# Performance work log

Hardware: AMD Instinct MI355X
Metric: run time of the kernel (lower is better)

The kernel has to match this reference:

```python
import jax, jax.numpy as jnp
import numpy as np
from jax import lax

PRE_NMS_TOPK = 6000
POST_NMS_TOPK = 1000
NMS_THRESH = 0.7
MIN_SIZE = 16.0


def setup_inputs() -> dict:
    key = jax.random.key(0)
    k1, k2, k3, k4 = jax.random.split(key, 4)
    N = 2_000_000
    H, W = 800, 1216
    images = jnp.zeros((1, H, W, 3), jnp.float32)  # only shape is used
    origin_sizes = jnp.ones((1, 2), jnp.float32)   # unused by forward math
    # synthesize valid anchor boxes (x1,y1,x2,y2) inside the image
    cxy = jax.random.uniform(k1, (N, 2), jnp.float32) * jnp.array([W, H], jnp.float32)
    wh = MIN_SIZE + jax.random.uniform(k2, (N, 2), jnp.float32) * 256.0
    anchors = jnp.concatenate([cxy - 0.5 * wh, cxy + 0.5 * wh], axis=1)
    bbox_deltas = 0.1 * jax.random.normal(k3, (N, 4), jnp.float32)
    logits = jax.random.normal(k4, (N, 1), jnp.float32)
    return {"images": images, "origin_sizes": origin_sizes, "anchors": anchors,
            "bbox_deltas": bbox_deltas, "logits": logits}


def _greedy_nms(boxes, valid_init):
    # boxes: [K,4] sorted by descending score; valid_init: [K] bool
    x1, y1, x2, y2 = boxes[:, 0], boxes[:, 1], boxes[:, 2], boxes[:, 3]
    areas = (x2 - x1) * (y2 - y1)

    def body(i, state):
        valid, keep = state
        idx = jnp.argmax(valid)          # first unsuppressed (boxes are score-sorted)
        ok = valid[idx]
        b = boxes[idx]
        xx1 = jnp.maximum(b[0], x1)
        yy1 = jnp.maximum(b[1], y1)
        xx2 = jnp.minimum(b[2], x2)
        yy2 = jnp.minimum(b[3], y2)
        inter = jnp.maximum(xx2 - xx1, 0.0) * jnp.maximum(yy2 - yy1, 0.0)
        iou = inter / (areas[idx] + areas - inter)
        valid = jnp.where(ok, valid & (iou <= NMS_THRESH), valid)  # self iou==1 suppresses idx
        keep = keep.at[i].set(jnp.where(ok, idx.astype(jnp.int32), -1))
        return valid, keep

    keep0 = jnp.full((POST_NMS_TOPK,), -1, jnp.int32)
    _, keep = lax.fori_loop(0, POST_NMS_TOPK, body, (valid_init, keep0))
    return keep


def reference(images, origin_sizes, anchors, bbox_deltas, logits):
    # ---- bbox delta decode ----
    wa = anchors[:, 2] - anchors[:, 0]
    ha = anchors[:, 3] - anchors[:, 1]
    xa = anchors[:, 0] + 0.5 * wa
    ya = anchors[:, 1] + 0.5 * ha
    x = bbox_deltas[:, 0] * wa + xa
    y = bbox_deltas[:, 1] * ha + ya
    w = jnp.exp(bbox_deltas[:, 2]) * wa
    h = jnp.exp(bbox_deltas[:, 3]) * ha
    # ---- clip to image ----
    height = jnp.float32(images.shape[1])
    width = jnp.float32(images.shape[2])
    x1 = jnp.clip(x - 0.5 * w, 0.0, width - 1.0)
    y1 = jnp.clip(y - 0.5 * h, 0.0, height - 1.0)
    x2 = jnp.clip(x + 0.5 * w, 0.0, width - 1.0)
    y2 = jnp.clip(y + 0.5 * h, 0.0, height - 1.0)
    proposals = jnp.stack([x1, y1, x2, y2], axis=1)  # [N,4]
    # ---- min-size filter (as score masking to stay static-shape) ----
    ok = ((x2 - x1) >= MIN_SIZE) & ((y2 - y1) >= MIN_SIZE)
    scores = jnp.where(ok, jax.nn.sigmoid(logits[:, 0]), -1.0)
    # ---- pre-NMS top-k ----
    top_scores, top_idx = lax.top_k(scores, PRE_NMS_TOPK)
    top_props = proposals[top_idx]           # [K,4]
    valid = top_scores >= 0.0
    # ---- greedy NMS (indices only; not differentiable) ----
    keep = _greedy_nms(lax.stop_gradient(top_props), valid)  # [post_nms_topk]
    kept_mask = keep >= 0
    out = jnp.where(kept_mask[:, None], top_props[jnp.maximum(keep, 0)], 0.0)
    return out  # [POST_NMS_TOPK, 4], zero rows where fewer than topk survive
```

## Files before the change

kernel.cpp:

```cpp
#include <hip/hip_runtime.h>
#include <hip/hip_bf16.h>
#include <stdint.h>

typedef unsigned int uint;
typedef unsigned long long ull;

#define NPRE   6000
#define NPOST  1000
#define NCH    94
#define MCAP   16384
#define IMG_W  1216.0f
#define IMG_H  800.0f

#define WS_KEYS    0
#define WS_HIST    8000000
#define WS_STATE   8001024
#define WS_K64     8001088
#define WS_IDX     8132160
#define WS_RANK    8197696
#define WS_SORTED  8263232
#define WS_MASK    8359488

__device__ __forceinline__ float exp_ref(float x) { return (float)exp((double)x); }

__device__ __forceinline__ float sigmoid_ref(float x) {
#pragma clang fp contract(off)
    float e = exp_ref(-x);
    float d = 1.0f + e;
    return 1.0f / d;
}

__device__ __forceinline__ bool decode_box(float4 a, float4 d,
                                           float& x1, float& y1, float& x2, float& y2) {
#pragma clang fp contract(off)
    float wa = a.z - a.x;
    float ha = a.w - a.y;
    float xa = a.x + 0.5f * wa;
    float ya = a.y + 0.5f * ha;
    float x  = d.x * wa + xa;
    float y  = d.y * ha + ya;
    float w  = exp_ref(d.z) * wa;
    float h  = exp_ref(d.w) * ha;
    x1 = fminf(fmaxf(x - 0.5f * w, 0.0f), IMG_W - 1.0f);
    y1 = fminf(fmaxf(y - 0.5f * h, 0.0f), IMG_H - 1.0f);
    x2 = fminf(fmaxf(x + 0.5f * w, 0.0f), IMG_W - 1.0f);
    y2 = fminf(fmaxf(y + 0.5f * h, 0.0f), IMG_H - 1.0f);
    return (x2 - x1 >= 16.0f) && (y2 - y1 >= 16.0f);
}

__device__ __forceinline__ bool sup_check(float ax1, float ay1, float ax2, float ay2, float aar,
                                          float bx1, float by1, float bx2, float by2, float bar) {
#pragma clang fp contract(off)
    float xx1 = fmaxf(ax1, bx1);
    float yy1 = fmaxf(ay1, by1);
    float xx2 = fminf(ax2, bx2);
    float yy2 = fminf(ay2, by2);
    float inter = fmaxf(xx2 - xx1, 0.0f) * fmaxf(yy2 - yy1, 0.0f);
    float uni = (aar + bar) - inter;
    return !(inter / uni <= 0.7f);
}

__global__ void k_init(uint* hist, uint* state, uint* rank, float4* sorted) {
    int t = blockIdx.x * blockDim.x + threadIdx.x;
    for (int i = t; i < MCAP; i += gridDim.x * blockDim.x) rank[i] = 0;
    if (t < 256) hist[t] = 0;
    if (t < 16)  state[t] = 0;
    if (t < 16)  sorted[NPRE + t] = make_float4(0.f, 0.f, 0.f, 0.f);
}

__global__ void k_decode_hist(const float4* __restrict__ A, const float4* __restrict__ D,
                              const float* __restrict__ L, uint* __restrict__ keys,
                              uint* __restrict__ hist, int N) {
    __shared__ uint h[256];
    int t = threadIdx.x;
    h[t] = 0;
    __syncthreads();
    for (int i = blockIdx.x * blockDim.x + t; i < N; i += gridDim.x * blockDim.x) {
        float x1, y1, x2, y2;
        bool ok = decode_box(A[i], D[i], x1, y1, x2, y2);
        uint key = 0u;
        if (ok) {
            float s = sigmoid_ref(L[i]);
            key = __float_as_uint(s) | 0x80000000u;
        }
        keys[i] = key;
        if ((key >> 24) == 0xBFu) atomicAdd(&h[(key >> 16) & 0xFFu], 1u);
    }
    __syncthreads();
    uint v = h[t];
    if (v) atomicAdd(&hist[t], v);
}

__global__ void k_scan256(const uint* __restrict__ hist, uint* state) {
    __shared__ uint S[256];
    int t = threadIdx.x;
    S[t] = hist[t];
    __syncthreads();
    for (int off = 1; off < 256; off <<= 1) {
        uint v = S[t] + ((t + off < 256) ? S[t + off] : 0u);
        __syncthreads();
        S[t] = v;
        __syncthreads();
    }
    uint Sincl = S[t];
    uint Sexcl = (t < 255) ? S[t + 1] : 0u;
    if (Sincl >= NPRE && Sexcl < NPRE) state[0] = (uint)t;
}

__global__ void k_compact16(const uint* __restrict__ keys, int N, uint* state,
                            ull* __restrict__ K64, int* __restrict__ idxArr) {
    int i = blockIdx.x * blockDim.x + threadIdx.x;
    int lane = threadIdx.x & 63;
    uint T16 = 0xBF00u | state[0];
    uint key = (i < N) ? keys[i] : 0u;
    bool push = (i < N) && ((key >> 16) >= T16);
    ull b = __ballot(push);
    if (!b) return;
    int ldr = __builtin_ctzll(b);
    uint base = 0;
    if (lane == ldr) base = atomicAdd(&state[1], (uint)__builtin_popcountll(b));
    base = (uint)__shfl((int)base, ldr, 64);
    if (push) {
        uint p = base + (uint)__builtin_popcountll(b & ((1ull << lane) - 1ull));
        if (p < MCAP) {
            K64[p] = ((ull)key << 32) | (uint)(~(uint)i);
            idxArr[p] = i;
        }
    }
}

__global__ __launch_bounds__(256) void k_rank(const ull* __restrict__ K64,
                                              const uint* __restrict__ state,
                                              uint* __restrict__ rank) {
    __shared__ ull tile[256];
    int M = (int)min(state[1], (uint)MCAP);
    if ((int)blockIdx.x * 256 >= M) return;
    int i = blockIdx.x * 256 + threadIdx.x;
    int W = (M + 7) / 8;
    int c0 = blockIdx.y * W;
    int c1 = min(c0 + W, M);
    ull mine = (i < M) ? K64[i] : 0ull;
    uint cnt = 0;
    for (int base = c0; base < c1; base += 256) {
        int j = base + threadIdx.x;
        tile[threadIdx.x] = (j < c1) ? K64[j] : 0ull;
        __syncthreads();
        int lim = min(256, c1 - base);
        for (int t = 0; t < lim; ++t) cnt += (tile[t] > mine);
        __syncthreads();
    }
    if (i < M && cnt) atomicAdd(&rank[i], cnt);
}

__global__ void k_scatter(const float4* __restrict__ A, const float4* __restrict__ D,
                          const uint* __restrict__ state, const uint* __restrict__ rank,
                          const int* __restrict__ idxArr, float4* __restrict__ sorted) {
    int i = blockIdx.x * blockDim.x + threadIdx.x;
    int M = (int)min(state[1], (uint)MCAP);
    if (i >= M) return;
    uint r = rank[i];
    if (r >= NPRE) return;
    int idx = idxArr[i];
    float x1, y1, x2, y2;
    decode_box(A[idx], D[idx], x1, y1, x2, y2);
    sorted[r] = make_float4(x1, y1, x2, y2);
}

__global__ __launch_bounds__(64) void k_mask(const float4* __restrict__ sorted,
                                             ull* __restrict__ mask) {
#pragma clang fp contract(off)
    if (blockIdx.x <= blockIdx.y) return;
    __shared__ float4 cb[64];
    __shared__ float  ca[64];
    int cw = blockIdx.x, rc = blockIdx.y, t = threadIdx.x;
    float4 b = sorted[cw * 64 + t];
    cb[t] = b;
    ca[t] = (b.z - b.x) * (b.w - b.y);
    __syncthreads();
    int row = rc * 64 + t;
    float4 rb = sorted[row];
    float  ra = (rb.z - rb.x) * (rb.w - rb.y);
    ull bits = 0;
    for (int j = 0; j < 64; ++j)
        if (sup_check(rb.x, rb.y, rb.z, rb.w, ra,
                      cb[j].x, cb[j].y, cb[j].z, cb[j].w, ca[j]))
            bits |= 1ull << j;
    mask[(size_t)row * NCH + cw] = bits;
}

__global__ __launch_bounds__(1024) void k_nms(const float4* __restrict__ sorted,
                                              const ull* __restrict__ mask,
                                              float* __restrict__ out) {
    int tid = threadIdx.x, lane = tid & 63, w = tid >> 6;
    __shared__ float kx1[NPOST], ky1[NPOST], kx2[NPOST], ky2[NPOST];
    __shared__ int   fIdx[64];
    __shared__ float cbx1[2][64], cby1[2][64], cbx2[2][64], cby2[2][64], cbar[2][64];
    __shared__ ull   intra[64];
    __shared__ uint  remLo[NCH], remHi[NCH];
    __shared__ int   kcS, nfS;

    for (int i = tid; i < NCH; i += 1024) { remLo[i] = 0; remHi[i] = 0; }
    if (tid < 64) {
#pragma clang fp contract(off)
        float4 b = sorted[tid];
        cbx1[0][tid] = b.x; cby1[0][tid] = b.y; cbx2[0][tid] = b.z; cby2[0][tid] = b.w;
        cbar[0][tid] = (b.z - b.x) * (b.w - b.y);
    }
    if (tid == 0) { kcS = 0; nfS = 0; }
    __syncthreads();

    int kc = 0, nf = 0;
    for (int c = 0; c < NCH; ++c) {
        int cur = c & 1;
        bool pf = (w == 15) && (c + 1 < NCH);
        float4 nb;
        if (pf) nb = sorted[(c + 1) * 64 + lane];
        float cx1 = cbx1[cur][lane], cy1 = cby1[cur][lane];
        float cx2 = cbx2[cur][lane], cy2 = cby2[cur][lane], car = cbar[cur][lane];
        for (int i2 = 0; i2 < 4; ++i2) {
            int r = w * 4 + i2;
            bool sup = sup_check(cbx1[cur][r], cby1[cur][r], cbx2[cur][r], cby2[cur][r], cbar[cur][r],
                                 cx1, cy1, cx2, cy2, car);
            ull bal = __ballot(sup);
            if (lane == 0) intra[r] = bal;
        }
        int nw = NCH - c;
        int pairs = nf * nw;
        for (int p = tid; p < pairs; p += 1024) {
            int k  = p / nw;
            int ww = c + (p - k * nw);
            ull m = mask[(size_t)fIdx[k] * NCH + ww];
            uint lo = (uint)m, hi = (uint)(m >> 32);
            if (lo) atomicOr(&remLo[ww], lo);
            if (hi) atomicOr(&remHi[ww], hi);
        }
        if (pf) {
#pragma clang fp contract(off)
            int nxt = cur ^ 1;
            cbx1[nxt][lane] = nb.x; cby1[nxt][lane] = nb.y;
            cbx2[nxt][lane] = nb.z; cby2[nxt][lane] = nb.w;
            cbar[nxt][lane] = (nb.z - nb.x) * (nb.w - nb.y);
        }
        __syncthreads();
        if (w == 0) {
            ull myrow = intra[lane];
            ull rm = ((ull)remHi[c] << 32) | (ull)remLo[c];
            if (c == NCH - 1) rm |= 0xFFFF000000000000ull;
            ull alive = ~rm;
            uint rlo = (uint)myrow, rhi = (uint)(myrow >> 32);
            ull keptbits = 0;
            int kcl = kc;
            while (alive && kcl < NPOST) {
                int j = __builtin_ctzll(alive);
                keptbits |= 1ull << j;
                kcl++;
                uint mlo = __builtin_amdgcn_readlane(rlo, j);
                uint mhi = __builtin_amdgcn_readlane(rhi, j);
                alive &= ~(((ull)mhi << 32) | (ull)mlo);
                alive &= ~(1ull << j);
            }
            if ((keptbits >> lane) & 1ull) {
                int r = kc + __builtin_popcountll(keptbits & ((1ull << lane) - 1ull));
                kx1[r] = cx1; ky1[r] = cy1; kx2[r] = cx2; ky2[r] = cy2;
                fIdx[r - kc] = c * 64 + lane;
            }
            if (lane == 0) { kcS = kcl; nfS = kcl - kc; }
        }
        __syncthreads();
        kc = kcS; nf = nfS;
        if (kc >= NPOST) break;
    }
    float4* o4 = (float4*)out;
    for (int r = tid; r < NPOST; r += 1024) {
        float4 b = make_float4(0.f, 0.f, 0.f, 0.f);
        if (r < kc) b = make_float4(kx1[r], ky1[r], kx2[r], ky2[r]);
        o4[r] = b;
    }
}

extern "C" void kernel_launch(void* const* d_in, const int* in_sizes, int n_in,
                              void* d_out, int out_size, void* d_ws, size_t ws_size,
                              hipStream_t stream) {
    const float4* A = (const float4*)d_in[2];
    const float4* D = (const float4*)d_in[3];
    const float*  L = (const float*)d_in[4];
    int N = in_sizes[4];

    char* ws = (char*)d_ws;
    uint*   keys   = (uint*)(ws + WS_KEYS);
    uint*   hist   = (uint*)(ws + WS_HIST);
    uint*   state  = (uint*)(ws + WS_STATE);
    ull*    K64    = (ull*)(ws + WS_K64);
    int*    idxArr = (int*)(ws + WS_IDX);
    uint*   rank   = (uint*)(ws + WS_RANK);
    float4* sorted = (float4*)(ws + WS_SORTED);
    ull*    mask   = (ull*)(ws + WS_MASK);
    float*  out    = (float*)d_out;

    int nblk = (N + 255) / 256;

    k_init<<<16, 1024, 0, stream>>>(hist, state, rank, sorted);
    k_decode_hist<<<2048, 256, 0, stream>>>(A, D, L, keys, hist, N);
    k_scan256<<<1, 256, 0, stream>>>(hist, state);
    k_compact16<<<nblk, 256, 0, stream>>>(keys, N, state, K64, idxArr);
    k_rank<<<dim3(64, 8), 256, 0, stream>>>(K64, state, rank);
    k_scatter<<<64, 256, 0, stream>>>(A, D, state, rank, idxArr, sorted);
    k_mask<<<dim3(NCH, NCH), 64, 0, stream>>>(sorted, mask);
    k_nms<<<1, 1024, 0, stream>>>(sorted, mask, out);
}
```

Before: 274.4 us.

## Process 128-box chunks in serial NMS and fold threshold scan into compaction

The single-block NMS loop now handles two 64-bit words (128 boxes) per iteration, which halves the number of serial chunk steps and barriers. Suppression of the current chunk by boxes kept in the previous chunk is computed directly from stored kept-box IoU checks rather than from the mask, so mask words only need ORing from the next chunk onward. Separately, the 256-bin histogram scan is recomputed inside every compaction block, removing one kernel launch at the cost of redundant per-block scan work. One risk is that state[0] is no longer written, so any later kernel that reads it would see a stale value.

Result: slower. 367.9 us (+34.1%).

```diff
diff --git a/kernel.cpp b/kernel.cpp
--- a/kernel.cpp
+++ b/kernel.cpp
@@ -7,7 +7,8 @@
 
 #define NPRE   6000
 #define NPOST  1000
-#define NCH    94
+#define NW     94
+#define CH2    47
 #define MCAP   16384
 #define IMG_W  1216.0f
 #define IMG_H  800.0f
@@ -91,9 +92,13 @@
     if (v) atomicAdd(&hist[t], v);
 }
 
-__global__ void k_scan256(const uint* __restrict__ hist, uint* state) {
+__global__ __launch_bounds__(256) void k_compact16(const uint* __restrict__ keys, int N,
+                                                   const uint* __restrict__ hist, uint* state,
+                                                   ull* __restrict__ K64, int* __restrict__ idxArr) {
     __shared__ uint S[256];
+    __shared__ uint t8s;
     int t = threadIdx.x;
+    if (t == 0) t8s = 0;
     S[t] = hist[t];
     __syncthreads();
     for (int off = 1; off < 256; off <<= 1) {
@@ -104,14 +109,12 @@
     }
     uint Sincl = S[t];
     uint Sexcl = (t < 255) ? S[t + 1] : 0u;
-    if (Sincl >= NPRE && Sexcl < NPRE) state[0] = (uint)t;
-}
-
-__global__ void k_compact16(const uint* __restrict__ keys, int N, uint* state,
-                            ull* __restrict__ K64, int* __restrict__ idxArr) {
-    int i = blockIdx.x * blockDim.x + threadIdx.x;
-    int lane = threadIdx.x & 63;
-    uint T16 = 0xBF00u | state[0];
+    if (Sincl >= NPRE && Sexcl < NPRE) t8s = (uint)t;
+    __syncthreads();
+    uint T16 = 0xBF00u | t8s;
+
+    int i = blockIdx.x * blockDim.x + t;
+    int lane = t & 63;
     uint key = (i < N) ? keys[i] : 0u;
     bool push = (i < N) && ((key >> 16) >= T16);
     ull b = __ballot(push);
@@ -185,84 +188,121 @@
         if (sup_check(rb.x, rb.y, rb.z, rb.w, ra,
                       cb[j].x, cb[j].y, cb[j].z, cb[j].w, ca[j]))
             bits |= 1ull << j;
-    mask[(size_t)row * NCH + cw] = bits;
+    mask[(size_t)row * NW + cw] = bits;
 }
 
 __global__ __launch_bounds__(1024) void k_nms(const float4* __restrict__ sorted,
                                               const ull* __restrict__ mask,
                                               float* __restrict__ out) {
     int tid = threadIdx.x, lane = tid & 63, w = tid >> 6;
-    __shared__ float kx1[NPOST], ky1[NPOST], kx2[NPOST], ky2[NPOST];
-    __shared__ int   fIdx[64];
-    __shared__ float cbx1[2][64], cby1[2][64], cbx2[2][64], cby2[2][64], cbar[2][64];
-    __shared__ ull   intra[64];
-    __shared__ uint  remLo[NCH], remHi[NCH];
+    __shared__ float kx1[NPOST], ky1[NPOST], kx2[NPOST], ky2[NPOST], kar[NPOST];
+    __shared__ int   fIdx[128];
+    __shared__ float cb[2][5][128];
+    __shared__ uint4 intraU[128];
+    __shared__ uint  remLo[NW], remHi[NW];
+    __shared__ ull   fp[16][2];
     __shared__ int   kcS, nfS;
 
-    for (int i = tid; i < NCH; i += 1024) { remLo[i] = 0; remHi[i] = 0; }
-    if (tid < 64) {
+    for (int i = tid; i < NW; i += 1024) { remLo[i] = 0; remHi[i] = 0; }
+    if (tid < 128) {
 #pragma clang fp contract(off)
         float4 b = sorted[tid];
-        cbx1[0][tid] = b.x; cby1[0][tid] = b.y; cbx2[0][tid] = b.z; cby2[0][tid] = b.w;
-        cbar[0][tid] = (b.z - b.x) * (b.w - b.y);
+        cb[0][0][tid] = b.x; cb[0][1][tid] = b.y; cb[0][2][tid] = b.z; cb[0][3][tid] = b.w;
+        cb[0][4][tid] = (b.z - b.x) * (b.w - b.y);
     }
     if (tid == 0) { kcS = 0; nfS = 0; }
     __syncthreads();
 
     int kc = 0, nf = 0;
-    for (int c = 0; c < NCH; ++c) {
-        int cur = c & 1;
-        bool pf = (w == 15) && (c + 1 < NCH);
+    for (int c = 0; c < CH2; ++c) {
+        int cur = c & 1, nxt = cur ^ 1;
+        bool pf = (w >= 14) && (c + 1 < CH2);
+        int pcol = (w - 14) * 64 + lane;
         float4 nb;
-        if (pf) nb = sorted[(c + 1) * 64 + lane];
-        float cx1 = cbx1[cur][lane], cy1 = cby1[cur][lane];
-        float cx2 = cbx2[cur][lane], cy2 = cby2[cur][lane], car = cbar[cur][lane];
-        for (int i2 = 0; i2 < 4; ++i2) {
-            int r = w * 4 + i2;
-            bool sup = sup_check(cbx1[cur][r], cby1[cur][r], cbx2[cur][r], cby2[cur][r], cbar[cur][r],
-                                 cx1, cy1, cx2, cy2, car);
-            ull bal = __ballot(sup);
-            if (lane == 0) intra[r] = bal;
-        }
-        int nw = NCH - c;
-        int pairs = nf * nw;
+        if (pf) nb = sorted[(c + 1) * 128 + pcol];
+        float cAx1 = cb[cur][0][lane],    cAy1 = cb[cur][1][lane];
+        float cAx2 = cb[cur][2][lane],    cAy2 = cb[cur][3][lane],    cAar = cb[cur][4][lane];
+        float cBx1 = cb[cur][0][64+lane], cBy1 = cb[cur][1][64+lane];
+        float cBx2 = cb[cur][2][64+lane], cBy2 = cb[cur][3][64+lane], cBar = cb[cur][4][64+lane];
+        for (int i2 = 0; i2 < 8; ++i2) {
+            int r = w * 8 + i2;
+            float rx1 = cb[cur][0][r], ry1 = cb[cur][1][r];
+            float rx2 = cb[cur][2][r], ry2 = cb[cur][3][r], rar = cb[cur][4][r];
+            ull balA = __ballot(sup_check(rx1, ry1, rx2, ry2, rar, cAx1, cAy1, cAx2, cAy2, cAar));
+            ull balB = __ballot(sup_check(rx1, ry1, rx2, ry2, rar, cBx1, cBy1, cBx2, cBy2, cBar));
+            if (lane == 0) intraU[r] = make_uint4((uint)balA, (uint)(balA >> 32),
+                                                  (uint)balB, (uint)(balB >> 32));
+        }
+        {
+            ull fA = 0, fB = 0;
+            for (int k = kc - nf + w; k < kc; k += 16) {
+                float px1 = kx1[k], py1 = ky1[k], px2 = kx2[k], py2 = ky2[k], par = kar[k];
+                fA |= __ballot(sup_check(px1, py1, px2, py2, par, cAx1, cAy1, cAx2, cAy2, cAar));
+                fB |= __ballot(sup_check(px1, py1, px2, py2, par, cBx1, cBy1, cBx2, cBy2, cBar));
+            }
+            if (lane == 0) { fp[w][0] = fA; fp[w][1] = fB; }
+        }
+        int w0 = 2 * c + 2;
+        int nwf = NW - w0;
+        int pairs = nf * nwf;
         for (int p = tid; p < pairs; p += 1024) {
-            int k  = p / nw;
-            int ww = c + (p - k * nw);
-            ull m = mask[(size_t)fIdx[k] * NCH + ww];
+            int k  = p / nwf;
+            int ww = w0 + (p - k * nwf);
+            ull m = mask[(size_t)fIdx[k] * NW + ww];
             uint lo = (uint)m, hi = (uint)(m >> 32);
             if (lo) atomicOr(&remLo[ww], lo);
             if (hi) atomicOr(&remHi[ww], hi);
         }
         if (pf) {
 #pragma clang fp contract(off)
-            int nxt = cur ^ 1;
-            cbx1[nxt][lane] = nb.x; cby1[nxt][lane] = nb.y;
-            cbx2[nxt][lane] = nb.z; cby2[nxt][lane] = nb.w;
-            cbar[nxt][lane] = (nb.z - nb.x) * (nb.w - nb.y);
+            cb[nxt][0][pcol] = nb.x; cb[nxt][1][pcol] = nb.y;
+            cb[nxt][2][pcol] = nb.z; cb[nxt][3][pcol] = nb.w;
+            cb[nxt][4][pcol] = (nb.z - nb.x) * (nb.w - nb.y);
         }
         __syncthreads();
         if (w == 0) {
-            ull myrow = intra[lane];
-            ull rm = ((ull)remHi[c] << 32) | (ull)remLo[c];
-            if (c == NCH - 1) rm |= 0xFFFF000000000000ull;
-            ull alive = ~rm;
-            uint rlo = (uint)myrow, rhi = (uint)(myrow >> 32);
-            ull keptbits = 0;
+            uint4 rA = intraU[lane];
+            uint4 rB = intraU[64 + lane];
+            ull fA = 0, fB = 0;
+            for (int i2 = 0; i2 < 16; ++i2) { fA |= fp[i2][0]; fB |= fp[i2][1]; }
+            ull alive0 = ~((((ull)remHi[2*c]   << 32) | (ull)remLo[2*c])   | fA);
+            ull alive1 = ~((((ull)remHi[2*c+1] << 32) | (ull)remLo[2*c+1]) | fB);
+            if (c == CH2 - 1) alive1 &= 0x0000FFFFFFFFFFFFull;
+            ull kept0 = 0, kept1 = 0;
             int kcl = kc;
-            while (alive && kcl < NPOST) {
-                int j = __builtin_ctzll(alive);
-                keptbits |= 1ull << j;
+            while ((alive0 | alive1) && kcl < NPOST) {
+                uint m0, m1, m2, m3;
+                if (alive0) {
+                    int j = __builtin_ctzll(alive0);
+                    m0 = __builtin_amdgcn_readlane(rA.x, j);
+                    m1 = __builtin_amdgcn_readlane(rA.y, j);
+                    m2 = __builtin_amdgcn_readlane(rA.z, j);
+                    m3 = __builtin_amdgcn_readlane(rA.w, j);
+                    kept0 |= 1ull << j;
+                    alive0 &= ~(1ull << j);
+                } else {
+                    int j = __builtin_ctzll(alive1);
+                    m0 = __builtin_amdgcn_readlane(rB.x, j);
+                    m1 = __builtin_amdgcn_readlane(rB.y, j);
+                    m2 = __builtin_amdgcn_readlane(rB.z, j);
+                    m3 = __builtin_amdgcn_readlane(rB.w, j);
+                    kept1 |= 1ull << j;
+                    alive1 &= ~(1ull << j);
+                }
                 kcl++;
-                uint mlo = __builtin_amdgcn_readlane(rlo, j);
-                uint mhi = __builtin_amdgcn_readlane(rhi, j);
-                alive &= ~(((ull)mhi << 32) | (ull)mlo);
-                alive &= ~(1ull << j);
+                alive0 &= ~(((ull)m1 << 32) | (ull)m0);
+                alive1 &= ~(((ull)m3 << 32) | (ull)m2);
             }
-            if ((keptbits >> lane) & 1ull) {
-                int r = kc + __builtin_popcountll(keptbits & ((1ull << lane) - 1ull));
-                kx1[r] = cx1; ky1[r] = cy1; kx2[r] = cx2; ky2[r] = cy2;
-                fIdx[r - kc] = c * 64 + lane;
+            int base1 = kc + __builtin_popcountll(kept0);
+            if ((kept0 >> lane) & 1ull) {
+                int r = kc + __builtin_popcountll(kept0 & ((1ull << lane) - 1ull));
+                kx1[r] = cAx1; ky1[r] = cAy1; kx2[r] = cAx2; ky2[r] = cAy2; kar[r] = cAar;
+                fIdx[r - kc] = c * 128 + lane;
+            }
+            if ((kept1 >> lane) & 1ull) {
+                int r = base1 + __builtin_popcountll(kept1 & ((1ull << lane) - 1ull));
+                kx1[r] = cBx1; ky1[r] = cBy1; kx2[r] = cBx2; ky2[r] = cBy2; kar[r] = cBar;
+                fIdx[r - kc] = c * 128 + 64 + lane;
             }
             if (lane == 0) { kcS = kcl; nfS = kcl - kc; }
         }
@@ -301,10 +341,9 @@
 
     k_init<<<16, 1024, 0, stream>>>(hist, state, rank, sorted);
     k_decode_hist<<<2048, 256, 0, stream>>>(A, D, L, keys, hist, N);
-    k_scan256<<<1, 256, 0, stream>>>(hist, state);
-    k_compact16<<<nblk, 256, 0, stream>>>(keys, N, state, K64, idxArr);
+    k_compact16<<<nblk, 256, 0, stream>>>(keys, N, hist, state, K64, idxArr);
     k_rank<<<dim3(64, 8), 256, 0, stream>>>(K64, state, rank);
     k_scatter<<<64, 256, 0, stream>>>(A, D, state, rank, idxArr, sorted);
-    k_mask<<<dim3(NCH, NCH), 64, 0, stream>>>(sorted, mask);
+    k_mask<<<dim3(NW, NW), 64, 0, stream>>>(sorted, mask);
     k_nms<<<1, 1024, 0, stream>>>(sorted, mask, out);
 }
```

## Fuse all pipeline stages into one cooperative persistent kernel with grid syncs

Applied to the files above, without the earlier changes.

Replaces the eight separate kernel launches (init, decode+histogram, scan, compaction, rank, scatter, IoU mask, NMS) with a single cooperative kernel of 256 blocks × 1024 threads, separated by grid-wide syncs. The scan is redundantly recomputed per block instead of in a separate launch, and the rank and mask stages are remapped onto the fixed grid. This removes per-launch overhead and inter-kernel gaps. In exchange it adds grid-sync costs, fixes occupancy at large blocks with heavy shared memory, and leaves the final NMS on a single block while the others exit.

After: 387.8 us. +41.3%, slower.

```diff
diff --git a/kernel.cpp b/kernel.cpp
--- a/kernel.cpp
+++ b/kernel.cpp
@@ -1,14 +1,19 @@
 #include <hip/hip_runtime.h>
-#include <hip/hip_bf16.h>
+#include <hip/hip_cooperative_groups.h>
 #include <stdint.h>
+
+namespace cg = cooperative_groups;
 
 typedef unsigned int uint;
 typedef unsigned long long ull;
 
 #define NPRE   6000
 #define NPOST  1000
-#define NCH    94
+#define NW     94
 #define MCAP   16384
+#define GRID   256
+#define BLK    1024
+#define GSTRIDE (GRID * BLK)
 #define IMG_W  1216.0f
 #define IMG_H  800.0f
 
@@ -60,233 +65,12 @@
     return !(inter / uni <= 0.7f);
 }
 
-__global__ void k_init(uint* hist, uint* state, uint* rank, float4* sorted) {
-    int t = blockIdx.x * blockDim.x + threadIdx.x;
-    for (int i = t; i < MCAP; i += gridDim.x * blockDim.x) rank[i] = 0;
-    if (t < 256) hist[t] = 0;
-    if (t < 16)  state[t] = 0;
-    if (t < 16)  sorted[NPRE + t] = make_float4(0.f, 0.f, 0.f, 0.f);
-}
-
-__global__ void k_decode_hist(const float4* __restrict__ A, const float4* __restrict__ D,
-                              const float* __restrict__ L, uint* __restrict__ keys,
-                              uint* __restrict__ hist, int N) {
-    __shared__ uint h[256];
-    int t = threadIdx.x;
-    h[t] = 0;
-    __syncthreads();
-    for (int i = blockIdx.x * blockDim.x + t; i < N; i += gridDim.x * blockDim.x) {
-        float x1, y1, x2, y2;
-        bool ok = decode_box(A[i], D[i], x1, y1, x2, y2);
-        uint key = 0u;
-        if (ok) {
-            float s = sigmoid_ref(L[i]);
-            key = __float_as_uint(s) | 0x80000000u;
-        }
-        keys[i] = key;
-        if ((key >> 24) == 0xBFu) atomicAdd(&h[(key >> 16) & 0xFFu], 1u);
-    }
-    __syncthreads();
-    uint v = h[t];
-    if (v) atomicAdd(&hist[t], v);
-}
-
-__global__ void k_scan256(const uint* __restrict__ hist, uint* state) {
-    __shared__ uint S[256];
-    int t = threadIdx.x;
-    S[t] = hist[t];
-    __syncthreads();
-    for (int off = 1; off < 256; off <<= 1) {
-        uint v = S[t] + ((t + off < 256) ? S[t + off] : 0u);
-        __syncthreads();
-        S[t] = v;
-        __syncthreads();
-    }
-    uint Sincl = S[t];
-    uint Sexcl = (t < 255) ? S[t + 1] : 0u;
-    if (Sincl >= NPRE && Sexcl < NPRE) state[0] = (uint)t;
-}
-
-__global__ void k_compact16(const uint* __restrict__ keys, int N, uint* state,
-                            ull* __restrict__ K64, int* __restrict__ idxArr) {
-    int i = blockIdx.x * blockDim.x + threadIdx.x;
-    int lane = threadIdx.x & 63;
-    uint T16 = 0xBF00u | state[0];
-    uint key = (i < N) ? keys[i] : 0u;
-    bool push = (i < N) && ((key >> 16) >= T16);
-    ull b = __ballot(push);
-    if (!b) return;
-    int ldr = __builtin_ctzll(b);
-    uint base = 0;
-    if (lane == ldr) base = atomicAdd(&state[1], (uint)__builtin_popcountll(b));
-    base = (uint)__shfl((int)base, ldr, 64);
-    if (push) {
-        uint p = base + (uint)__builtin_popcountll(b & ((1ull << lane) - 1ull));
-        if (p < MCAP) {
-            K64[p] = ((ull)key << 32) | (uint)(~(uint)i);
-            idxArr[p] = i;
-        }
-    }
-}
-
-__global__ __launch_bounds__(256) void k_rank(const ull* __restrict__ K64,
-                                              const uint* __restrict__ state,
-                                              uint* __restrict__ rank) {
-    __shared__ ull tile[256];
-    int M = (int)min(state[1], (uint)MCAP);
-    if ((int)blockIdx.x * 256 >= M) return;
-    int i = blockIdx.x * 256 + threadIdx.x;
-    int W = (M + 7) / 8;
-    int c0 = blockIdx.y * W;
-    int c1 = min(c0 + W, M);
-    ull mine = (i < M) ? K64[i] : 0ull;
-    uint cnt = 0;
-    for (int base = c0; base < c1; base += 256) {
-        int j = base + threadIdx.x;
-        tile[threadIdx.x] = (j < c1) ? K64[j] : 0ull;
-        __syncthreads();
-        int lim = min(256, c1 - base);
-        for (int t = 0; t < lim; ++t) cnt += (tile[t] > mine);
-        __syncthreads();
-    }
-    if (i < M && cnt) atomicAdd(&rank[i], cnt);
-}
-
-__global__ void k_scatter(const float4* __restrict__ A, const float4* __restrict__ D,
-                          const uint* __restrict__ state, const uint* __restrict__ rank,
-                          const int* __restrict__ idxArr, float4* __restrict__ sorted) {
-    int i = blockIdx.x * blockDim.x + threadIdx.x;
-    int M = (int)min(state[1], (uint)MCAP);
-    if (i >= M) return;
-    uint r = rank[i];
-    if (r >= NPRE) return;
-    int idx = idxArr[i];
-    float x1, y1, x2, y2;
-    decode_box(A[idx], D[idx], x1, y1, x2, y2);
-    sorted[r] = make_float4(x1, y1, x2, y2);
-}
-
-__global__ __launch_bounds__(64) void k_mask(const float4* __restrict__ sorted,
-                                             ull* __restrict__ mask) {
-#pragma clang fp contract(off)
-    if (blockIdx.x <= blockIdx.y) return;
-    __shared__ float4 cb[64];
-    __shared__ float  ca[64];
-    int cw = blockIdx.x, rc = blockIdx.y, t = threadIdx.x;
-    float4 b = sorted[cw * 64 + t];
-    cb[t] = b;
-    ca[t] = (b.z - b.x) * (b.w - b.y);
-    __syncthreads();
-    int row = rc * 64 + t;
-    float4 rb = sorted[row];
-    float  ra = (rb.z - rb.x) * (rb.w - rb.y);
-    ull bits = 0;
-    for (int j = 0; j < 64; ++j)
-        if (sup_check(rb.x, rb.y, rb.z, rb.w, ra,
-                      cb[j].x, cb[j].y, cb[j].z, cb[j].w, ca[j]))
-            bits |= 1ull << j;
-    mask[(size_t)row * NCH + cw] = bits;
-}
-
-__global__ __launch_bounds__(1024) void k_nms(const float4* __restrict__ sorted,
-                                              const ull* __restrict__ mask,
-                                              float* __restrict__ out) {
-    int tid = threadIdx.x, lane = tid & 63, w = tid >> 6;
-    __shared__ float kx1[NPOST], ky1[NPOST], kx2[NPOST], ky2[NPOST];
-    __shared__ int   fIdx[64];
-    __shared__ float cbx1[2][64], cby1[2][64], cbx2[2][64], cby2[2][64], cbar[2][64];
-    __shared__ ull   intra[64];
-    __shared__ uint  remLo[NCH], remHi[NCH];
-    __shared__ int   kcS, nfS;
-
-    for (int i = tid; i < NCH; i += 1024) { remLo[i] = 0; remHi[i] = 0; }
-    if (tid < 64) {
-#pragma clang fp contract(off)
-        float4 b = sorted[tid];
-        cbx1[0][tid] = b.x; cby1[0][tid] = b.y; cbx2[0][tid] = b.z; cby2[0][tid] = b.w;
-        cbar[0][tid] = (b.z - b.x) * (b.w - b.y);
-    }
-    if (tid == 0) { kcS = 0; nfS = 0; }
-    __syncthreads();
-
-    int kc = 0, nf = 0;
-    for (int c = 0; c < NCH; ++c) {
-        int cur = c & 1;
-        bool pf = (w == 15) && (c + 1 < NCH);
-        float4 nb;
-        if (pf) nb = sorted[(c + 1) * 64 + lane];
-        float cx1 = cbx1[cur][lane], cy1 = cby1[cur][lane];
-        float cx2 = cbx2[cur][lane], cy2 = cby2[cur][lane], car = cbar[cur][lane];
-        for (int i2 = 0; i2 < 4; ++i2) {
-            int r = w * 4 + i2;
-            bool sup = sup_check(cbx1[cur][r], cby1[cur][r], cbx2[cur][r], cby2[cur][r], cbar[cur][r],
-                                 cx1, cy1, cx2, cy2, car);
-            ull bal = __ballot(sup);
-            if (lane == 0) intra[r] = bal;
-        }
-        int nw = NCH - c;
-        int pairs = nf * nw;
-        for (int p = tid; p < pairs; p += 1024) {
-            int k  = p / nw;
-            int ww = c + (p - k * nw);
-            ull m = mask[(size_t)fIdx[k] * NCH + ww];
-            uint lo = (uint)m, hi = (uint)(m >> 32);
-            if (lo) atomicOr(&remLo[ww], lo);
-            if (hi) atomicOr(&remHi[ww], hi);
-        }
-        if (pf) {
-#pragma clang fp contract(off)
-            int nxt = cur ^ 1;
-            cbx1[nxt][lane] = nb.x; cby1[nxt][lane] = nb.y;
-            cbx2[nxt][lane] = nb.z; cby2[nxt][lane] = nb.w;
-            cbar[nxt][lane] = (nb.z - nb.x) * (nb.w - nb.y);
-        }
-        __syncthreads();
-        if (w == 0) {
-            ull myrow = intra[lane];
-            ull rm = ((ull)remHi[c] << 32) | (ull)remLo[c];
-            if (c == NCH - 1) rm |= 0xFFFF000000000000ull;
-            ull alive = ~rm;
-            uint rlo = (uint)myrow, rhi = (uint)(myrow >> 32);
-            ull keptbits = 0;
-            int kcl = kc;
-            while (alive && kcl < NPOST) {
-                int j = __builtin_ctzll(alive);
-                keptbits |= 1ull << j;
-                kcl++;
-                uint mlo = __builtin_amdgcn_readlane(rlo, j);
-                uint mhi = __builtin_amdgcn_readlane(rhi, j);
-                alive &= ~(((ull)mhi << 32) | (ull)mlo);
-                alive &= ~(1ull << j);
-            }
-            if ((keptbits >> lane) & 1ull) {
-                int r = kc + __builtin_popcountll(keptbits & ((1ull << lane) - 1ull));
-                kx1[r] = cx1; ky1[r] = cy1; kx2[r] = cx2; ky2[r] = cy2;
-                fIdx[r - kc] = c * 64 + lane;
-            }
-            if (lane == 0) { kcS = kcl; nfS = kcl - kc; }
-        }
-        __syncthreads();
-        kc = kcS; nf = nfS;
-        if (kc >= NPOST) break;
-    }
-    float4* o4 = (float4*)out;
-    for (int r = tid; r < NPOST; r += 1024) {
-        float4 b = make_float4(0.f, 0.f, 0.f, 0.f);
-        if (r < kc) b = make_float4(kx1[r], ky1[r], kx2[r], ky2[r]);
-        o4[r] = b;
-    }
-}
-
-extern "C" void kernel_launch(void* const* d_in, const int* in_sizes, int n_in,
-                              void* d_out, int out_size, void* d_ws, size_t ws_size,
-                              hipStream_t stream) {
-    const float4* A = (const float4*)d_in[2];
-    const float4* D = (const float4*)d_in[3];
-    const float*  L = (const float*)d_in[4];
-    int N = in_sizes[4];
-
-    char* ws = (char*)d_ws;
+__global__ __launch_bounds__(BLK, 4) void k_mega(const float4* __restrict__ A,
+                                                 const float4* __restrict__ D,
+                                                 const float* __restrict__ L,
+                                                 char* __restrict__ ws,
+                                                 float* __restrict__ out, int N) {
+    cg::grid_group gg = cg::this_grid();
     uint*   keys   = (uint*)(ws + WS_KEYS);
     uint*   hist   = (uint*)(ws + WS_HIST);
     uint*   state  = (uint*)(ws + WS_STATE);
@@ -295,16 +79,237 @@
     uint*   rank   = (uint*)(ws + WS_RANK);
     float4* sorted = (float4*)(ws + WS_SORTED);
     ull*    mask   = (ull*)(ws + WS_MASK);
-    float*  out    = (float*)d_out;
-
-    int nblk = (N + 255) / 256;
-
-    k_init<<<16, 1024, 0, stream>>>(hist, state, rank, sorted);
-    k_decode_hist<<<2048, 256, 0, stream>>>(A, D, L, keys, hist, N);
-    k_scan256<<<1, 256, 0, stream>>>(hist, state);
-    k_compact16<<<nblk, 256, 0, stream>>>(keys, N, state, K64, idxArr);
-    k_rank<<<dim3(64, 8), 256, 0, stream>>>(K64, state, rank);
-    k_scatter<<<64, 256, 0, stream>>>(A, D, state, rank, idxArr, sorted);
-    k_mask<<<dim3(NCH, NCH), 64, 0, stream>>>(sorted, mask);
-    k_nms<<<1, 1024, 0, stream>>>(sorted, mask, out);
-}
+
+    int tid = threadIdx.x, bid = blockIdx.x;
+    int gtid = bid * BLK + tid;
+    int lane = tid & 63;
+
+    __shared__ uint h[256];
+    __shared__ uint Sscan[256];
+    __shared__ uint t8s;
+    __shared__ ull  tileS[BLK];
+    __shared__ float4 mcb[16][64];
+    __shared__ float  mca[16][64];
+    __shared__ float kx1[NPOST], ky1[NPOST], kx2[NPOST], ky2[NPOST];
+    __shared__ int   fIdx[64];
+    __shared__ float cbx1[2][64], cby1[2][64], cbx2[2][64], cby2[2][64], cbar[2][64];
+    __shared__ ull   intra[64];
+    __shared__ uint  remLo[NW], remHi[NW];
+    __shared__ int   kcS, nfS;
+
+    for (int i = gtid; i < MCAP; i += GSTRIDE) rank[i] = 0;
+    if (gtid < 256) hist[gtid] = 0;
+    if (gtid >= 256 && gtid < 272) state[gtid - 256] = 0;
+    if (gtid >= 272 && gtid < 288) sorted[NPRE + gtid - 272] = make_float4(0.f, 0.f, 0.f, 0.f);
+    gg.sync();
+
+    if (tid < 256) h[tid] = 0;
+    __syncthreads();
+    for (int i = gtid; i < N; i += GSTRIDE) {
+        float x1, y1, x2, y2;
+        bool ok = decode_box(A[i], D[i], x1, y1, x2, y2);
+        uint key = 0u;
+        if (ok) {
+            float s = sigmoid_ref(L[i]);
+            key = __float_as_uint(s) | 0x80000000u;
+        }
+        keys[i] = key;
+        if ((key >> 24) == 0xBFu) atomicAdd(&h[(key >> 16) & 0xFFu], 1u);
+    }
+    __syncthreads();
+    if (tid < 256 && h[tid]) atomicAdd(&hist[tid], h[tid]);
+    gg.sync();
+
+    if (tid == 0) t8s = 0;
+    if (tid < 256) Sscan[tid] = hist[tid];
+    __syncthreads();
+    for (int off = 1; off < 256; off <<= 1) {
+        uint v = 0;
+        if (tid < 256) v = Sscan[tid] + ((tid + off < 256) ? Sscan[tid + off] : 0u);
+        __syncthreads();
+        if (tid < 256) Sscan[tid] = v;
+        __syncthreads();
+    }
+    if (tid < 256) {
+        uint Sincl = Sscan[tid];
+        uint Sexcl = (tid < 255) ? Sscan[tid + 1] : 0u;
+        if (Sincl >= NPRE && Sexcl < NPRE) t8s = (uint)tid;
+    }
+    __syncthreads();
+    {
+        uint T16 = 0xBF00u | t8s;
+        int nIter = (N + GSTRIDE - 1) / GSTRIDE;
+        for (int it = 0; it < nIter; ++it) {
+            int i = it * GSTRIDE + gtid;
+            uint key = (i < N) ? keys[i] : 0u;
+            bool push = (i < N) && ((key >> 16) >= T16);
+            ull b = __ballot(push);
+            if (b) {
+                int ldr = __builtin_ctzll(b);
+                uint base = 0;
+                if (lane == ldr) base = atomicAdd(&state[1], (uint)__builtin_popcountll(b));
+                base = (uint)__shfl((int)base, ldr, 64);
+                if (push) {
+                    uint p = base + (uint)__builtin_popcountll(b & ((1ull << lane) - 1ull));
+                    if (p < MCAP) {
+                        K64[p] = ((ull)key << 32) | (uint)(~(uint)i);
+                        idxArr[p] = i;
+                    }
+                }
+            }
+        }
+    }
+    gg.sync();
+
+    int M = (int)min(state[1], (uint)MCAP);
+
+    {
+        int rb = bid & 15, sl = bid >> 4;
+        int i = rb * BLK + tid;
+        int W = (M + 15) / 16;
+        int c0 = sl * W;
+        int c1 = min(c0 + W, M);
+        ull mine = (i < M) ? K64[i] : 0ull;
+        uint cnt = 0;
+        for (int base = c0; base < c1; base += BLK) {
+            int j = base + tid;
+            tileS[tid] = (j < c1) ? K64[j] : 0ull;
+            __syncthreads();
+            int lim = min(BLK, c1 - base);
+            for (int t2 = 0; t2 < lim; ++t2) cnt += (tileS[t2] > mine);
+            __syncthreads();
+        }
+        if (i < M && cnt) atomicAdd(&rank[i], cnt);
+    }
+    gg.sync();
+
+    for (int i = gtid; i < M; i += GSTRIDE) {
+        uint r = rank[i];
+        if (r < NPRE) {
+            int idx = idxArr[i];
+            float x1, y1, x2, y2;
+            decode_box(A[idx], D[idx], x1, y1, x2, y2);
+            sorted[r] = make_float4(x1, y1, x2, y2);
+        }
+    }
+    gg.sync();
+
+    {
+#pragma clang fp contract(off)
+        int sub = tid >> 6;
+        for (int p = bid * 16 + sub; p < NW * NW; p += GRID * 16) {
+            int rc = p / NW, cw = p - rc * NW;
+            if (cw <= rc) continue;
+            float4 b = sorted[cw * 64 + lane];
+            mcb[sub][lane] = b;
+            mca[sub][lane] = (b.z - b.x) * (b.w - b.y);
+            int row = rc * 64 + lane;
+            float4 rb = sorted[row];
+            float  ra = (rb.z - rb.x) * (rb.w - rb.y);
+            ull bits = 0;
+            for (int j = 0; j < 64; ++j)
+                if (sup_check(rb.x, rb.y, rb.z, rb.w, ra,
+                              mcb[sub][j].x, mcb[sub][j].y, mcb[sub][j].z, mcb[sub][j].w,
+                              mca[sub][j]))
+                    bits |= 1ull << j;
+            mask[(size_t)row * NW + cw] = bits;
+        }
+    }
+    gg.sync();
+
+    if (bid != 0) return;
+    {
+        int wv = tid >> 6;
+        for (int i = tid; i < NW; i += BLK) { remLo[i] = 0; remHi[i] = 0; }
+        if (tid < 64) {
+#pragma clang fp contract(off)
+            float4 b = sorted[tid];
+            cbx1[0][tid] = b.x; cby1[0][tid] = b.y; cbx2[0][tid] = b.z; cby2[0][tid] = b.w;
+            cbar[0][tid] = (b.z - b.x) * (b.w - b.y);
+        }
+        if (tid == 0) { kcS = 0; nfS = 0; }
+        __syncthreads();
+
+        int kc = 0, nf = 0;
+        for (int c = 0; c < NW; ++c) {
+            int cur = c & 1;
+            bool pf = (wv == 15) && (c + 1 < NW);
+            float4 nb;
+            if (pf) nb = sorted[(c + 1) * 64 + lane];
+            float cx1 = cbx1[cur][lane], cy1 = cby1[cur][lane];
+            float cx2 = cbx2[cur][lane], cy2 = cby2[cur][lane], car = cbar[cur][lane];
+            for (int i2 = 0; i2 < 4; ++i2) {
+                int r = wv * 4 + i2;
+                bool sup = sup_check(cbx1[cur][r], cby1[cur][r], cbx2[cur][r], cby2[cur][r],
+                                     cbar[cur][r], cx1, cy1, cx2, cy2, car);
+                ull bal = __ballot(sup);
+                if (lane == 0) intra[r] = bal;
+            }
+            int nw2 = NW - c;
+            int pairs = nf * nw2;
+            for (int p = tid; p < pairs; p += BLK) {
+                int k  = p / nw2;
+                int ww = c + (p - k * nw2);
+                ull m = mask[(size_t)fIdx[k] * NW + ww];
+                uint lo = (uint)m, hi = (uint)(m >> 32);
+                if (lo) atomicOr(&remLo[ww], lo);
+                if (hi) atomicOr(&remHi[ww], hi);
+            }
+            if (pf) {
+#pragma clang fp contract(off)
+                int nxt = cur ^ 1;
+                cbx1[nxt][lane] = nb.x; cby1[nxt][lane] = nb.y;
+                cbx2[nxt][lane] = nb.z; cby2[nxt][lane] = nb.w;
+                cbar[nxt][lane] = (nb.z - nb.x) * (nb.w - nb.y);
+            }
+            __syncthreads();
+            if (wv == 0) {
+                ull myrow = intra[lane];
+                ull rm = ((ull)remHi[c] << 32) | (ull)remLo[c];
+                if (c == NW - 1) rm |= 0xFFFF000000000000ull;
+                ull alive = ~rm;
+                uint rlo = (uint)myrow, rhi = (uint)(myrow >> 32);
+                ull keptbits = 0;
+                int kcl = kc;
+                while (alive && kcl < NPOST) {
+                    int j = __builtin_ctzll(alive);
+                    keptbits |= 1ull << j;
+                    kcl++;
+                    uint mlo = __builtin_amdgcn_readlane(rlo, j);
+                    uint mhi = __builtin_amdgcn_readlane(rhi, j);
+                    alive &= ~(((ull)mhi << 32) | (ull)mlo);
+                    alive &= ~(1ull << j);
+                }
+                if ((keptbits >> lane) & 1ull) {
+                    int r = kc + __builtin_popcountll(keptbits & ((1ull << lane) - 1ull));
+                    kx1[r] = cx1; ky1[r] = cy1; kx2[r] = cx2; ky2[r] = cy2;
+                    fIdx[r - kc] = c * 64 + lane;
+                }
+                if (lane == 0) { kcS = kcl; nfS = kcl - kc; }
+            }
+            __syncthreads();
+            kc = kcS; nf = nfS;
+            if (kc >= NPOST) break;
+        }
+        float4* o4 = (float4*)out;
+        for (int r = tid; r < NPOST; r += BLK) {
+            float4 b = make_float4(0.f, 0.f, 0.f, 0.f);
+            if (r < kc) b = make_float4(kx1[r], ky1[r], kx2[r], ky2[r]);
+            o4[r] = b;
+        }
+    }
+}
+
+extern "C" void kernel_launch(void* const* d_in, const int* in_sizes, int n_in,
+                              void* d_out, int out_size, void* d_ws, size_t ws_size,
+                              hipStream_t stream) {
+    const float4* A = (const float4*)d_in[2];
+    const float4* D = (const float4*)d_in[3];
+    const float*  L = (const float*)d_in[4];
+    int N = in_sizes[4];
+    char* ws = (char*)d_ws;
+    float* out = (float*)d_out;
+
+    void* args[6] = { (void*)&A, (void*)&D, (void*)&L, (void*)&ws, (void*)&out, (void*)&N };
+    hipLaunchCooperativeKernel((void*)k_mega, dim3(GRID), dim3(BLK), args, 0, stream);
+}
```

## Fuse threshold scan into compaction and shorten NMS critical path with direct IoU

Applied to the files above, without the earlier changes.

The single-block histogram scan is folded into the compaction kernel: every block recomputes the 256-bin threshold in shared memory, which removes one launch and the round-trip through global state. The NMS kernel drops to 256 threads. Boxes kept in the previous chunk are now tested against the current chunk with direct IoU checks, while their mask rows are OR-ed only into later chunks, so each chunk no longer waits on the mask merge. In exchange, every compaction block repeats the scan, and `state[0]` is no longer written in case any later kernel reads it.

Measured after the change: 430.3 us. +56.8%, slower.

```diff
diff --git a/kernel.cpp b/kernel.cpp
--- a/kernel.cpp
+++ b/kernel.cpp
@@ -7,7 +7,7 @@
 
 #define NPRE   6000
 #define NPOST  1000
-#define NCH    94
+#define NW     94
 #define MCAP   16384
 #define IMG_W  1216.0f
 #define IMG_H  800.0f
@@ -91,9 +91,13 @@
     if (v) atomicAdd(&hist[t], v);
 }
 
-__global__ void k_scan256(const uint* __restrict__ hist, uint* state) {
+__global__ __launch_bounds__(256) void k_compact16(const uint* __restrict__ keys, int N,
+                                                   const uint* __restrict__ hist, uint* state,
+                                                   ull* __restrict__ K64, int* __restrict__ idxArr) {
     __shared__ uint S[256];
+    __shared__ uint t8s;
     int t = threadIdx.x;
+    if (t == 0) t8s = 0;
     S[t] = hist[t];
     __syncthreads();
     for (int off = 1; off < 256; off <<= 1) {
@@ -104,14 +108,12 @@
     }
     uint Sincl = S[t];
     uint Sexcl = (t < 255) ? S[t + 1] : 0u;
-    if (Sincl >= NPRE && Sexcl < NPRE) state[0] = (uint)t;
-}
-
-__global__ void k_compact16(const uint* __restrict__ keys, int N, uint* state,
-                            ull* __restrict__ K64, int* __restrict__ idxArr) {
-    int i = blockIdx.x * blockDim.x + threadIdx.x;
-    int lane = threadIdx.x & 63;
-    uint T16 = 0xBF00u | state[0];
+    if (Sincl >= NPRE && Sexcl < NPRE) t8s = (uint)t;
+    __syncthreads();
+    uint T16 = 0xBF00u | t8s;
+
+    int i = blockIdx.x * blockDim.x + t;
+    int lane = t & 63;
     uint key = (i < N) ? keys[i] : 0u;
     bool push = (i < N) && ((key >> 16) >= T16);
     ull b = __ballot(push);
@@ -185,21 +187,22 @@
         if (sup_check(rb.x, rb.y, rb.z, rb.w, ra,
                       cb[j].x, cb[j].y, cb[j].z, cb[j].w, ca[j]))
             bits |= 1ull << j;
-    mask[(size_t)row * NCH + cw] = bits;
-}
-
-__global__ __launch_bounds__(1024) void k_nms(const float4* __restrict__ sorted,
-                                              const ull* __restrict__ mask,
-                                              float* __restrict__ out) {
+    mask[(size_t)row * NW + cw] = bits;
+}
+
+__global__ __launch_bounds__(256) void k_nms(const float4* __restrict__ sorted,
+                                             const ull* __restrict__ mask,
+                                             float* __restrict__ out) {
     int tid = threadIdx.x, lane = tid & 63, w = tid >> 6;
-    __shared__ float kx1[NPOST], ky1[NPOST], kx2[NPOST], ky2[NPOST];
+    __shared__ float kx1[NPOST], ky1[NPOST], kx2[NPOST], ky2[NPOST], kar[NPOST];
     __shared__ int   fIdx[64];
     __shared__ float cbx1[2][64], cby1[2][64], cbx2[2][64], cby2[2][64], cbar[2][64];
     __shared__ ull   intra[64];
-    __shared__ uint  remLo[NCH], remHi[NCH];
+    __shared__ ull   fpW[4];
+    __shared__ uint  remLo[NW], remHi[NW];
     __shared__ int   kcS, nfS;
 
-    for (int i = tid; i < NCH; i += 1024) { remLo[i] = 0; remHi[i] = 0; }
+    for (int i = tid; i < NW; i += 256) { remLo[i] = 0; remHi[i] = 0; }
     if (tid < 64) {
 #pragma clang fp contract(off)
         float4 b = sorted[tid];
@@ -210,26 +213,35 @@
     __syncthreads();
 
     int kc = 0, nf = 0;
-    for (int c = 0; c < NCH; ++c) {
+    for (int c = 0; c < NW; ++c) {
         int cur = c & 1;
-        bool pf = (w == 15) && (c + 1 < NCH);
+        bool pf = (w == 3) && (c + 1 < NW);
         float4 nb;
         if (pf) nb = sorted[(c + 1) * 64 + lane];
         float cx1 = cbx1[cur][lane], cy1 = cby1[cur][lane];
         float cx2 = cbx2[cur][lane], cy2 = cby2[cur][lane], car = cbar[cur][lane];
-        for (int i2 = 0; i2 < 4; ++i2) {
-            int r = w * 4 + i2;
-            bool sup = sup_check(cbx1[cur][r], cby1[cur][r], cbx2[cur][r], cby2[cur][r], cbar[cur][r],
-                                 cx1, cy1, cx2, cy2, car);
+        for (int i2 = 0; i2 < 16; ++i2) {
+            int r = w * 16 + i2;
+            bool sup = sup_check(cbx1[cur][r], cby1[cur][r], cbx2[cur][r], cby2[cur][r],
+                                 cbar[cur][r], cx1, cy1, cx2, cy2, car);
             ull bal = __ballot(sup);
             if (lane == 0) intra[r] = bal;
         }
-        int nw = NCH - c;
-        int pairs = nf * nw;
-        for (int p = tid; p < pairs; p += 1024) {
-            int k  = p / nw;
-            int ww = c + (p - k * nw);
-            ull m = mask[(size_t)fIdx[k] * NCH + ww];
+        {
+            ull f = 0;
+            for (int k = kc - nf + w; k < kc; k += 4) {
+                f |= __ballot(sup_check(kx1[k], ky1[k], kx2[k], ky2[k], kar[k],
+                                        cx1, cy1, cx2, cy2, car));
+            }
+            if (lane == 0) fpW[w] = f;
+        }
+        int w0 = c + 1;
+        int nwf = NW - w0;
+        int pairs = nf * nwf;
+        for (int p = tid; p < pairs; p += 256) {
+            int k  = p / nwf;
+            int ww = w0 + (p - k * nwf);
+            ull m = mask[(size_t)fIdx[k] * NW + ww];
             uint lo = (uint)m, hi = (uint)(m >> 32);
             if (lo) atomicOr(&remLo[ww], lo);
             if (hi) atomicOr(&remHi[ww], hi);
@@ -244,24 +256,25 @@
         __syncthreads();
         if (w == 0) {
             ull myrow = intra[lane];
-            ull rm = ((ull)remHi[c] << 32) | (ull)remLo[c];
-            if (c == NCH - 1) rm |= 0xFFFF000000000000ull;
+            ull rm = (((ull)remHi[c] << 32) | (ull)remLo[c]) | fpW[0] | fpW[1] | fpW[2] | fpW[3];
+            if (c == NW - 1) rm |= 0xFFFF000000000000ull;
             ull alive = ~rm;
             uint rlo = (uint)myrow, rhi = (uint)(myrow >> 32);
             ull keptbits = 0;
             int kcl = kc;
             while (alive && kcl < NPOST) {
                 int j = __builtin_ctzll(alive);
-                keptbits |= 1ull << j;
+                int js = __builtin_amdgcn_readfirstlane(j);
+                keptbits |= 1ull << js;
                 kcl++;
-                uint mlo = __builtin_amdgcn_readlane(rlo, j);
-                uint mhi = __builtin_amdgcn_readlane(rhi, j);
+                uint mlo = __builtin_amdgcn_readlane(rlo, js);
+                uint mhi = __builtin_amdgcn_readlane(rhi, js);
                 alive &= ~(((ull)mhi << 32) | (ull)mlo);
-                alive &= ~(1ull << j);
+                alive &= ~(1ull << js);
             }
             if ((keptbits >> lane) & 1ull) {
                 int r = kc + __builtin_popcountll(keptbits & ((1ull << lane) - 1ull));
-                kx1[r] = cx1; ky1[r] = cy1; kx2[r] = cx2; ky2[r] = cy2;
+                kx1[r] = cx1; ky1[r] = cy1; kx2[r] = cx2; ky2[r] = cy2; kar[r] = car;
                 fIdx[r - kc] = c * 64 + lane;
             }
             if (lane == 0) { kcS = kcl; nfS = kcl - kc; }
@@ -271,7 +284,7 @@
         if (kc >= NPOST) break;
     }
     float4* o4 = (float4*)out;
-    for (int r = tid; r < NPOST; r += 1024) {
+    for (int r = tid; r < NPOST; r += 256) {
         float4 b = make_float4(0.f, 0.f, 0.f, 0.f);
         if (r < kc) b = make_float4(kx1[r], ky1[r], kx2[r], ky2[r]);
         o4[r] = b;
@@ -301,10 +314,9 @@
 
     k_init<<<16, 1024, 0, stream>>>(hist, state, rank, sorted);
     k_decode_hist<<<2048, 256, 0, stream>>>(A, D, L, keys, hist, N);
-    k_scan256<<<1, 256, 0, stream>>>(hist, state);
-    k_compact16<<<nblk, 256, 0, stream>>>(keys, N, state, K64, idxArr);
+    k_compact16<<<nblk, 256, 0, stream>>>(keys, N, hist, state, K64, idxArr);
     k_rank<<<dim3(64, 8), 256, 0, stream>>>(K64, state, rank);
     k_scatter<<<64, 256, 0, stream>>>(A, D, state, rank, idxArr, sorted);
-    k_mask<<<dim3(NCH, NCH), 64, 0, stream>>>(sorted, mask);
-    k_nms<<<1, 1024, 0, stream>>>(sorted, mask, out);
-}
+    k_mask<<<dim3(NW, NW), 64, 0, stream>>>(sorted, mask);
+    k_nms<<<1, 256, 0, stream>>>(sorted, mask, out);
+}
```
